# Optimization experiments

Hardware: AMD Instinct MI355X
Metric: run time of the kernel (lower is better)

The kernel has to match this reference:

```python
import jax, jax.numpy as jnp
import numpy as np

N_NODES = 50000   # num graph nodes
N_EDGES = 800000  # avg degree 16
D = 96            # in_channels == out_channels (residual aggr_out + x)


def setup_inputs() -> dict:
    key = jax.random.key(0)
    k0, k1, k2, k3, k4 = jax.random.split(key, 5)
    x = jax.random.normal(k0, (N_NODES, D), dtype=jnp.float32)
    edge_index = jax.random.randint(k1, (2, N_EDGES), 0, N_NODES)  # [2,E]: row0=src(j), row1=dst(i)
    edge_weight = jax.random.uniform(k2, (N_EDGES,), dtype=jnp.float32)
    pagerank = jax.random.uniform(k3, (N_NODES,), dtype=jnp.float32)
    # nn.Linear(in_channels, out_channels) params
    W = jax.random.normal(k4, (D, D), dtype=jnp.float32) / np.sqrt(D).astype(np.float32)
    b = jnp.zeros((D,), dtype=jnp.float32)
    return {"x": x, "edge_index": edge_index, "edge_weight": edge_weight,
            "pagerank": pagerank, "W": W, "b": b}


def reference(x, edge_index, edge_weight, pagerank, W, b):
    # CGCConv (PyG MessagePassing, aggr='add', flow source_to_target):
    #   message: edge_weight * x_j * pagerank_j   (gather from source nodes)
    #   aggregate: scatter-add to destination nodes
    #   update: Linear(aggr_out + x)
    src = edge_index[0]
    dst = edge_index[1]
    # [E, D] messages: per-edge gather-multiply
    msgs = edge_weight[:, None] * x[src] * pagerank[src][:, None]
    aggr = jax.ops.segment_sum(msgs, dst, num_segments=x.shape[0])  # [N, D]
    return (aggr + x) @ W.T + b
```

## Files before the change

kernel.cpp:

```cpp
#include <hip/hip_runtime.h>


constexpr int NN = 50000;
constexpr int NE = 800000;
constexpr int DD = 96;
constexpr int CAPN = 64;
constexpr int NEBLK = (NE + 511) / 512;
constexpr int NCVT = (NN * DD / 4 + 511) / 512;

using s8v = __attribute__((ext_vector_type(8))) short;
using f4v = __attribute__((ext_vector_type(4))) float;

__device__ inline unsigned short f2bf(float f) {
    unsigned u = __float_as_uint(f);
    return (unsigned short)((u + 0x7FFFu + ((u >> 16) & 1u)) >> 16);
}
__device__ inline float bfh(unsigned short v) {
    return __uint_as_float((unsigned)v << 16);
}

__global__ __launch_bounds__(512) void k_bin(const int* __restrict__ src,
                                             const int* __restrict__ dst,
                                             const float* __restrict__ ew,
                                             const float* __restrict__ pr,
                                             int* __restrict__ cnt,
                                             unsigned* __restrict__ ep,
                                             const float4* __restrict__ x4,
                                             ushort4* __restrict__ y16v,
                                             const float* __restrict__ W,
                                             unsigned short* __restrict__ wfrag) {
    int tid = threadIdx.x;
    int blk = blockIdx.x;
    if (blk >= NEBLK) {
        int ci = blk - NEBLK;
        if (ci < NCVT) {
            int i = ci * 512 + tid;
            if (i < NN * DD / 4) {
                float4 v = x4[i];
                y16v[i] = make_ushort4(f2bf(v.x), f2bf(v.y), f2bf(v.z), f2bf(v.w));
            }
        } else {
            for (int i = tid; i < 18 * 512; i += 512) {
                int f = i >> 9, r = i & 511;
                int lane = r >> 3, j = r & 7;
                int ks = f / 6, nt = f - 6 * ks;
                int n = nt * 16 + (lane & 15);
                int k = ks * 32 + (lane >> 4) * 8 + j;
                wfrag[i] = f2bf(W[n * DD + k]);
            }
        }
        return;
    }
    int e = blk * 512 + tid;
    if (e >= NE) return;
    int d = dst[e];
    int s = src[e];
    float c = ew[e] * pr[s];
    unsigned cbf = f2bf(c);
    int slot = atomicAdd(&cnt[d], 1);
    if (slot < CAPN)
        ep[((size_t)d << 6) + slot] = (unsigned)(s & 0xffff) | (cbf << 16);
}

__global__ __launch_bounds__(256) void k_pull(const ushort4* __restrict__ y16v,
                                              const float4* __restrict__ x4,
                                              const int* __restrict__ cnt,
                                              const unsigned* __restrict__ ep,
                                              ushort4* __restrict__ io16v) {
    int g = blockIdx.x * 8 + (threadIdx.x >> 5);
    int lane = threadIdx.x & 31;
    if (g >= NN || lane >= 24) return;
    int beg = g << 6;
    int deg = cnt[g];
    float ax = 0.f, ay = 0.f, az = 0.f, aw = 0.f;
    int k = 0;
    for (; k + 8 <= deg; k += 8) {
        unsigned e[8];
        #pragma unroll
        for (int j = 0; j < 8; j++) e[j] = ep[beg + k + j];
        ushort4 u[8];
        #pragma unroll
        for (int j = 0; j < 8; j++)
            u[j] = y16v[(size_t)(e[j] & 0xffff) * 24 + lane];
        #pragma unroll
        for (int j = 0; j < 8; j++) {
            float c = bfh((unsigned short)(e[j] >> 16));
            ax += c * bfh(u[j].x);
            ay += c * bfh(u[j].y);
            az += c * bfh(u[j].z);
            aw += c * bfh(u[j].w);
        }
    }
    for (; k + 4 <= deg; k += 4) {
        unsigned e[4];
        #pragma unroll
        for (int j = 0; j < 4; j++) e[j] = ep[beg + k + j];
        ushort4 u[4];
        #pragma unroll
        for (int j = 0; j < 4; j++)
            u[j] = y16v[(size_t)(e[j] & 0xffff) * 24 + lane];
        #pragma unroll
        for (int j = 0; j < 4; j++) {
            float c = bfh((unsigned short)(e[j] >> 16));
            ax += c * bfh(u[j].x);
            ay += c * bfh(u[j].y);
            az += c * bfh(u[j].z);
            aw += c * bfh(u[j].w);
        }
    }
    for (; k < deg; k++) {
        unsigned e = ep[beg + k];
        ushort4 u = y16v[(size_t)(e & 0xffff) * 24 + lane];
        float c = bfh((unsigned short)(e >> 16));
        ax += c * bfh(u.x);
        ay += c * bfh(u.y);
        az += c * bfh(u.z);
        aw += c * bfh(u.w);
    }
    float4 xn = x4[(size_t)g * 24 + lane];
    io16v[(size_t)g * 24 + lane] = make_ushort4(f2bf(ax + xn.x), f2bf(ay + xn.y),
                                                f2bf(az + xn.z), f2bf(aw + xn.w));
}

__global__ __launch_bounds__(256) void k_gemm(const unsigned short* __restrict__ io16,
                                              const unsigned short* __restrict__ wfrag,
                                              const float* __restrict__ b,
                                              float* __restrict__ out) {
    int tid = threadIdx.x;
    int wave = tid >> 6, lane = tid & 63;
    int quad = lane >> 4, m16 = lane & 15;
    int r0 = blockIdx.x * 64 + wave * 16;
    int rowa = r0 + m16;
    if (rowa >= NN) rowa = NN - 1;

    const s8v* wf = (const s8v*)wfrag;

    f4v acc[6];
    #pragma unroll
    for (int nt = 0; nt < 6; nt++) acc[nt] = (f4v){0.f, 0.f, 0.f, 0.f};

    #pragma unroll
    for (int ks = 0; ks < 3; ks++) {
        s8v a = *(const s8v*)(io16 + (size_t)rowa * DD + ks * 32 + quad * 8);
        #pragma unroll
        for (int nt = 0; nt < 6; nt++) {
            s8v bb = wf[(ks * 6 + nt) * 64 + lane];
            acc[nt] = __builtin_amdgcn_mfma_f32_16x16x32_bf16(a, bb, acc[nt], 0, 0, 0);
        }
    }

    #pragma unroll
    for (int nt = 0; nt < 6; nt++) {
        float bias = b[nt * 16 + m16];
        #pragma unroll
        for (int reg = 0; reg < 4; reg++) {
            int rr = r0 + quad * 4 + reg;
            if (rr < NN)
                out[(size_t)rr * DD + nt * 16 + m16] = acc[nt][reg] + bias;
        }
    }
}

extern "C" void kernel_launch(void* const* d_in, const int* in_sizes, int n_in,
                              void* d_out, int out_size, void* d_ws, size_t ws_size,
                              hipStream_t stream) {
    const float* x  = (const float*)d_in[0];
    const int*   ei = (const int*)d_in[1];
    const float* ew = (const float*)d_in[2];
    const float* pr = (const float*)d_in[3];
    const float* W  = (const float*)d_in[4];
    const float* b  = (const float*)d_in[5];
    float* out = (float*)d_out;

    unsigned* ep = (unsigned*)d_ws;
    unsigned short* y16 = (unsigned short*)(ep + (size_t)NN * CAPN);
    int* cnt = (int*)(y16 + (size_t)NN * DD);
    unsigned short* io16 = (unsigned short*)(cnt + NN);
    unsigned short* wfrag = io16 + (size_t)NN * DD;

    const int* src = ei;
    const int* dst = ei + NE;

    hipMemsetAsync(cnt, 0, NN * sizeof(int), stream);
    k_bin<<<NEBLK + NCVT + 1, 512, 0, stream>>>(src, dst, ew, pr, cnt, ep,
                                                (const float4*)x, (ushort4*)y16,
                                                W, wfrag);
    k_pull<<<(NN + 7) / 8, 256, 0, stream>>>((const ushort4*)y16, (const float4*)x,
                                             cnt, ep, (ushort4*)io16);
    k_gemm<<<(NN + 63) / 64, 256, 0, stream>>>(io16, wfrag, b, out);
}
```

Before: 164.1 us.

## Replace per-node CSR binning with bucketed block-sort and LDS-atomic aggregation

Edges are locally sorted inside each prep block by destination bucket of 128 nodes, then scattered into per-bucket staging arrays with one global atomic per bucket instead of one per edge. Aggregation then runs one block per bucket, accumulating messages into a shared-memory tile with LDS float atomics before the residual add and bf16 conversion. This removes the per-node global atomics and the 64-slot-per-node capacity limit. In exchange, only 391 aggregation blocks run, LDS atomics contend, and each bucket holds at most 2560 edges.

```diff
diff --git a/kernel.cpp b/kernel.cpp
--- a/kernel.cpp
+++ b/kernel.cpp
@@ -4,12 +4,16 @@
 constexpr int NN = 50000;
 constexpr int NE = 800000;
 constexpr int DD = 96;
-constexpr int CAPN = 64;
-constexpr int NEBLK = (NE + 511) / 512;
+constexpr int NB = 391;
+constexpr int BKN = 128;
+constexpr int CAPB = 2560;
+constexpr int EPB = 4096;
+constexpr int NBLK = (NE + EPB - 1) / EPB;
 constexpr int NCVT = (NN * DD / 4 + 511) / 512;
 
 using s8v = __attribute__((ext_vector_type(8))) short;
 using f4v = __attribute__((ext_vector_type(4))) float;
+using u16x8 = __attribute__((ext_vector_type(8))) unsigned short;
 
 __device__ inline unsigned short f2bf(float f) {
     unsigned u = __float_as_uint(f);
@@ -18,21 +22,25 @@
 __device__ inline float bfh(unsigned short v) {
     return __uint_as_float((unsigned)v << 16);
 }
-
-__global__ __launch_bounds__(512) void k_bin(const int* __restrict__ src,
-                                             const int* __restrict__ dst,
-                                             const float* __restrict__ ew,
-                                             const float* __restrict__ pr,
-                                             int* __restrict__ cnt,
-                                             unsigned* __restrict__ ep,
-                                             const float4* __restrict__ x4,
-                                             ushort4* __restrict__ y16v,
-                                             const float* __restrict__ W,
-                                             unsigned short* __restrict__ wfrag) {
+__device__ inline unsigned long long pack_e(int meta, float c) {
+    return (unsigned long long)(unsigned)meta |
+           ((unsigned long long)(unsigned)__float_as_uint(c) << 32);
+}
+
+__global__ __launch_bounds__(512) void k_prep(const int* __restrict__ src,
+                                              const int* __restrict__ dst,
+                                              const float* __restrict__ ew,
+                                              const float* __restrict__ pr,
+                                              int* __restrict__ cur1,
+                                              unsigned long long* __restrict__ stage,
+                                              const float4* __restrict__ x4,
+                                              ushort4* __restrict__ y16v,
+                                              const float* __restrict__ W,
+                                              unsigned short* __restrict__ wfrag) {
     int tid = threadIdx.x;
     int blk = blockIdx.x;
-    if (blk >= NEBLK) {
-        int ci = blk - NEBLK;
+    if (blk >= NBLK) {
+        int ci = blk - NBLK;
         if (ci < NCVT) {
             int i = ci * 512 + tid;
             if (i < NN * DD / 4) {
@@ -51,75 +59,126 @@
         }
         return;
     }
-    int e = blk * 512 + tid;
-    if (e >= NE) return;
-    int d = dst[e];
-    int s = src[e];
-    float c = ew[e] * pr[s];
-    unsigned cbf = f2bf(c);
-    int slot = atomicAdd(&cnt[d], 1);
-    if (slot < CAPN)
-        ep[((size_t)d << 6) + slot] = (unsigned)(s & 0xffff) | (cbf << 16);
-}
-
-__global__ __launch_bounds__(256) void k_pull(const ushort4* __restrict__ y16v,
+    int wv = tid >> 6, ln = tid & 63;
+    __shared__ int h[8][512];
+    __shared__ int tot[512];
+    __shared__ int sc[512];
+    __shared__ int gb[512];
+    __shared__ int wsum[8];
+    __shared__ unsigned long long sorted[EPB];
+
+    for (int i = ln; i < 512; i += 64) h[wv][i] = 0;
+    int base = blockIdx.x * EPB;
+    int n = min(EPB, NE - base);
+
+    unsigned long long ent[8]; int bkt[8]; int lrk[8];
+    #pragma unroll
+    for (int j = 0; j < 8; j++) {
+        int e = base + j * 512 + tid;
+        bkt[j] = -1;
+        if (e < NE) {
+            int d = dst[e];
+            int s = src[e];
+            float c = ew[e] * pr[s];
+            int bk = d >> 7;
+            bkt[j] = bk;
+            lrk[j] = atomicAdd(&h[wv][bk], 1);
+            ent[j] = pack_e(s | ((d & 127) << 16) | (bk << 23), c);
+        }
+    }
+    __syncthreads();
+    int run = 0;
+    #pragma unroll
+    for (int w = 0; w < 8; w++) { int v = h[w][tid]; h[w][tid] = run; run += v; }
+    tot[tid] = run;
+    int scv = run;
+    #pragma unroll
+    for (int o = 1; o < 64; o <<= 1) {
+        int t = __shfl_up(scv, o);
+        if (ln >= o) scv += t;
+    }
+    if (ln == 63) wsum[wv] = scv;
+    __syncthreads();
+    int add = 0;
+    #pragma unroll
+    for (int w = 0; w < 8; w++) add += (w < wv) ? wsum[w] : 0;
+    sc[tid] = scv + add;
+    if (tid < NB)
+        gb[tid] = tot[tid] ? atomicAdd(&cur1[tid], tot[tid]) : 0;
+    __syncthreads();
+    #pragma unroll
+    for (int j = 0; j < 8; j++)
+        if (bkt[j] >= 0)
+            sorted[sc[bkt[j]] - tot[bkt[j]] + h[wv][bkt[j]] + lrk[j]] = ent[j];
+    __syncthreads();
+    for (int i = tid; i < n; i += 512) {
+        unsigned long long e = sorted[i];
+        int bk = ((int)(e >> 23)) & 0x1ff;
+        stage[(size_t)bk * CAPB + gb[bk] + (i - (sc[bk] - tot[bk]))] = e;
+    }
+}
+
+__global__ __launch_bounds__(512) void k_aggr(const unsigned long long* __restrict__ stage,
+                                              const int* __restrict__ cur1,
+                                              const unsigned short* __restrict__ y16,
                                               const float4* __restrict__ x4,
-                                              const int* __restrict__ cnt,
-                                              const unsigned* __restrict__ ep,
-                                              ushort4* __restrict__ io16v) {
-    int g = blockIdx.x * 8 + (threadIdx.x >> 5);
-    int lane = threadIdx.x & 31;
-    if (g >= NN || lane >= 24) return;
-    int beg = g << 6;
-    int deg = cnt[g];
-    float ax = 0.f, ay = 0.f, az = 0.f, aw = 0.f;
-    int k = 0;
-    for (; k + 8 <= deg; k += 8) {
-        unsigned e[8];
-        #pragma unroll
-        for (int j = 0; j < 8; j++) e[j] = ep[beg + k + j];
-        ushort4 u[8];
-        #pragma unroll
-        for (int j = 0; j < 8; j++)
-            u[j] = y16v[(size_t)(e[j] & 0xffff) * 24 + lane];
-        #pragma unroll
-        for (int j = 0; j < 8; j++) {
-            float c = bfh((unsigned short)(e[j] >> 16));
-            ax += c * bfh(u[j].x);
-            ay += c * bfh(u[j].y);
-            az += c * bfh(u[j].z);
-            aw += c * bfh(u[j].w);
-        }
-    }
-    for (; k + 4 <= deg; k += 4) {
-        unsigned e[4];
-        #pragma unroll
-        for (int j = 0; j < 4; j++) e[j] = ep[beg + k + j];
-        ushort4 u[4];
-        #pragma unroll
-        for (int j = 0; j < 4; j++)
-            u[j] = y16v[(size_t)(e[j] & 0xffff) * 24 + lane];
-        #pragma unroll
-        for (int j = 0; j < 4; j++) {
-            float c = bfh((unsigned short)(e[j] >> 16));
-            ax += c * bfh(u[j].x);
-            ay += c * bfh(u[j].y);
-            az += c * bfh(u[j].z);
-            aw += c * bfh(u[j].w);
-        }
-    }
-    for (; k < deg; k++) {
-        unsigned e = ep[beg + k];
-        ushort4 u = y16v[(size_t)(e & 0xffff) * 24 + lane];
-        float c = bfh((unsigned short)(e >> 16));
-        ax += c * bfh(u.x);
-        ay += c * bfh(u.y);
-        az += c * bfh(u.z);
-        aw += c * bfh(u.w);
-    }
-    float4 xn = x4[(size_t)g * 24 + lane];
-    io16v[(size_t)g * 24 + lane] = make_ushort4(f2bf(ax + xn.x), f2bf(ay + xn.y),
-                                                f2bf(az + xn.z), f2bf(aw + xn.w));
+                                              u16x8* __restrict__ io16v8) {
+    __shared__ float aggr[BKN][DD];
+    int tid = threadIdx.x;
+    int wv = tid >> 6, ln = tid & 63;
+    int b = blockIdx.x;
+    size_t base = (size_t)b * CAPB;
+    int n = cur1[b];
+
+    float* af = &aggr[0][0];
+    for (int s = tid; s < BKN * DD; s += 512) af[s] = 0.f;
+    __syncthreads();
+
+    int ch = 2 * ln;
+    int i = wv;
+    for (; i + 8 < n; i += 16) {
+        unsigned long long e0 = stage[base + i];
+        unsigned long long e1 = stage[base + i + 8];
+        if (ln < 48) {
+            unsigned p0 = *(const unsigned*)(y16 + (size_t)(e0 & 0xffff) * DD + ch);
+            unsigned p1 = *(const unsigned*)(y16 + (size_t)(e1 & 0xffff) * DD + ch);
+            int d0 = ((int)(e0 >> 16)) & 0x7f;
+            int d1 = ((int)(e1 >> 16)) & 0x7f;
+            float c0 = __uint_as_float((unsigned)(e0 >> 32));
+            float c1 = __uint_as_float((unsigned)(e1 >> 32));
+            atomicAdd(&aggr[d0][ch],     c0 * bfh((unsigned short)p0));
+            atomicAdd(&aggr[d0][ch + 1], c0 * bfh((unsigned short)(p0 >> 16)));
+            atomicAdd(&aggr[d1][ch],     c1 * bfh((unsigned short)p1));
+            atomicAdd(&aggr[d1][ch + 1], c1 * bfh((unsigned short)(p1 >> 16)));
+        }
+    }
+    for (; i < n; i += 8) {
+        unsigned long long e = stage[base + i];
+        if (ln < 48) {
+            unsigned pp = *(const unsigned*)(y16 + (size_t)(e & 0xffff) * DD + ch);
+            int dl = ((int)(e >> 16)) & 0x7f;
+            float c = __uint_as_float((unsigned)(e >> 32));
+            atomicAdd(&aggr[dl][ch],     c * bfh((unsigned short)pp));
+            atomicAdd(&aggr[dl][ch + 1], c * bfh((unsigned short)(pp >> 16)));
+        }
+    }
+    __syncthreads();
+
+    for (int s = tid; s < BKN * 12; s += 512) {
+        int nl = s / 12, q = s - nl * 12;
+        int g = (b << 7) + nl;
+        if (g < NN) {
+            float4 xl = x4[(size_t)g * 24 + q * 2];
+            float4 xh = x4[(size_t)g * 24 + q * 2 + 1];
+            const float* a = &aggr[nl][q * 8];
+            u16x8 o;
+            o[0] = f2bf(a[0] + xl.x); o[1] = f2bf(a[1] + xl.y);
+            o[2] = f2bf(a[2] + xl.z); o[3] = f2bf(a[3] + xl.w);
+            o[4] = f2bf(a[4] + xh.x); o[5] = f2bf(a[5] + xh.y);
+            o[6] = f2bf(a[6] + xh.z); o[7] = f2bf(a[7] + xh.w);
+            io16v8[(size_t)g * 12 + q] = o;
+        }
+    }
 }
 
 __global__ __launch_bounds__(256) void k_gemm(const unsigned short* __restrict__ io16,
@@ -172,20 +231,20 @@
     const float* b  = (const float*)d_in[5];
     float* out = (float*)d_out;
 
-    unsigned* ep = (unsigned*)d_ws;
-    unsigned short* y16 = (unsigned short*)(ep + (size_t)NN * CAPN);
-    int* cnt = (int*)(y16 + (size_t)NN * DD);
-    unsigned short* io16 = (unsigned short*)(cnt + NN);
+    unsigned long long* stage = (unsigned long long*)d_ws;
+    unsigned short* y16 = (unsigned short*)(stage + (size_t)NB * CAPB);
+    int* cur1 = (int*)(y16 + (size_t)NN * DD);
+    unsigned short* io16 = (unsigned short*)(cur1 + 512);
     unsigned short* wfrag = io16 + (size_t)NN * DD;
 
     const int* src = ei;
     const int* dst = ei + NE;
 
-    hipMemsetAsync(cnt, 0, NN * sizeof(int), stream);
-    k_bin<<<NEBLK + NCVT + 1, 512, 0, stream>>>(src, dst, ew, pr, cnt, ep,
+    hipMemsetAsync(cur1, 0, NB * sizeof(int), stream);
+    k_prep<<<NBLK + NCVT + 1, 512, 0, stream>>>(src, dst, ew, pr, cur1, stage,
                                                 (const float4*)x, (ushort4*)y16,
                                                 W, wfrag);
-    k_pull<<<(NN + 7) / 8, 256, 0, stream>>>((const ushort4*)y16, (const float4*)x,
-                                             cnt, ep, (ushort4*)io16);
+    k_aggr<<<NB, 512, 0, stream>>>(stage, cur1, y16, (const float4*)x,
+                                   (u16x8*)io16);
     k_gemm<<<(NN + 63) / 64, 256, 0, stream>>>(io16, wfrag, b, out);
 }
```

Result: slower. 623.9 us (+280.3%).
